# Performance work log

Hardware: AMD Instinct MI355X
Metric: run time of the kernel (lower is better)

Reference implementation:

```python
import jax, jax.numpy as jnp
import numpy as np

EPS = 1e-12  # torch F.normalize eps

def _l2norm(t, axis):
    n = jnp.linalg.norm(t, axis=axis, keepdims=True)
    return t / jnp.maximum(n, EPS)

def setup_inputs() -> dict:
    key = jax.random.key(0)
    ks = jax.random.split(key, 7)
    B, L, D, F, K = 16, 128, 512, 1024, 16
    return {
        "x": jax.random.normal(ks[0], (B, L, D), jnp.float32),
        "W_gate_basis": jax.random.normal(ks[1], (K, D, F), jnp.float32) * (1.0 / np.sqrt(D)),
        "W_up_basis": jax.random.normal(ks[2], (K, D, F), jnp.float32) * (1.0 / np.sqrt(D)),
        "W_down_basis": jax.random.normal(ks[3], (K, F, D), jnp.float32) * (1.0 / np.sqrt(F)),
        "token_coef1": jax.random.normal(ks[4], (L, K), jnp.float32),
        "token_coef2": jax.random.normal(ks[5], (L, K), jnp.float32),
        "token_coef3": jax.random.normal(ks[6], (L, K), jnp.float32),
        "u_scale_param": jnp.ones((1, F), jnp.float32),
        "v_scale_param": jnp.ones((1, F), jnp.float32),
    }

def reference(x, W_gate_basis, W_up_basis, W_down_basis,
              token_coef1, token_coef2, token_coef3,
              u_scale_param, v_scale_param):
    D = x.shape[-1]
    c1 = jax.nn.softmax(token_coef1, axis=-1)
    c2 = jax.nn.softmax(token_coef2, axis=-1)
    c3 = jax.nn.softmax(token_coef3, axis=-1)
    # per-token weights [L, D, F] / [L, F, D]
    W_gate = jnp.einsum('lk,kio->lio', c1, W_gate_basis)
    W_up = jnp.einsum('lk,kio->lio', c2, W_up_basis)
    W_down = jnp.einsum('lk,koj->loj', c3, W_down_basis)
    W_gate = _l2norm(W_gate, axis=1)   # normalize over input dim D
    W_up = _l2norm(W_up, axis=1)
    W_down = _l2norm(W_down, axis=1)   # normalize over hidden dim F
    u = jnp.einsum('bld,ldf->blf', x, W_gate)
    v = jnp.einsum('bld,ldf->blf', x, W_up)
    u_scale = jnp.abs(u_scale_param) * 1.0
    v_scale = jnp.abs(v_scale_param) * jnp.sqrt(jnp.float32(D))
    h = jax.nn.silu(v_scale * v) * (u_scale * u)
    out = jnp.einsum('blf,lfd->bld', h, W_down)
    return _l2norm(out, axis=-1)
```

## Files before the change

kernel.cpp:

```cpp
#include <hip/hip_runtime.h>
#include <hip/hip_bf16.h>
#include <cmath>


typedef _Float16 half8 __attribute__((ext_vector_type(8)));
typedef _Float16 half4 __attribute__((ext_vector_type(4)));
typedef float    f32x4 __attribute__((ext_vector_type(4)));

#define MFMA_F16 __builtin_amdgcn_mfma_f32_16x16x32_f16

static constexpr size_t OFF_P1 = 0;
static constexpr size_t OFF_P2 = 16777216;
static constexpr size_t OFF_P3 = 33554432;
static constexpr size_t OFF_HP = 50331648;
static constexpr size_t WS_FAST = OFF_HP + 4194304;

__global__ __launch_bounds__(256) void prep_basis_all(
    const float* __restrict__ wg, const float* __restrict__ wu,
    const float* __restrict__ wd,
    _Float16* __restrict__ P1, _Float16* __restrict__ P2,
    _Float16* __restrict__ P3)
{
    int z = blockIdx.y;
    const float* src = (z == 0) ? wg : (z == 1) ? wu : wd;
    _Float16*    dst = (z == 0) ? P1 : (z == 1) ? P2 : P3;
    int A  = (z == 2) ? 1024 : 512;
    int Bd = (z == 2) ? 512 : 1024;
    int nb = Bd >> 6;
    int a0 = (blockIdx.x / nb) * 4;
    int b0 = (blockIdx.x % nb) * 64;

    __shared__ __align__(16) float S[16 * 257];
    int tid = threadIdx.x;
#pragma unroll
    for (int k = 0; k < 16; ++k)
        S[k * 257 + tid] =
            src[(size_t)k * A * Bd + (size_t)(a0 + (tid >> 6)) * Bd + b0 + (tid & 63)];
    __syncthreads();

    int a = tid >> 6, b = tid & 63;
    const float* col = &S[tid];
    half8 v0, v1;
#pragma unroll
    for (int k = 0; k < 8; ++k) v0[k] = (_Float16)col[k * 257];
#pragma unroll
    for (int k = 0; k < 8; ++k) v1[k] = (_Float16)col[(k + 8) * 257];
    _Float16* out = dst + ((size_t)(a0 + a) * Bd + (b0 + b)) * 16;
    *(half8*)out       = v0;
    *(half8*)(out + 8) = v1;
}

__global__ __launch_bounds__(256) void up_fast(
    const _Float16* __restrict__ P1, const _Float16* __restrict__ P2,
    const float* __restrict__ x,
    const float* __restrict__ tc1, const float* __restrict__ tc2,
    const float* __restrict__ usp, const float* __restrict__ vsp,
    _Float16* __restrict__ Hp)
{
    int lg = blockIdx.x >> 6;
    int f0 = (blockIdx.x & 63) * 16;
    int tid = threadIdx.x;
    int w = tid >> 6, lane = tid & 63;
    int n = lane & 15, kc = lane >> 4;

    __shared__ __align__(16) _Float16 Bh[2][32 * 264];
    __shared__ __align__(16) _Float16 Wt[2][16 * 648];
    __shared__ float CN[2 * 256];

    if (tid < 32) {
        int s = tid >> 4, ll = tid & 15;
        const float* row = (s ? tc2 : tc1) + (size_t)(lg * 16 + ll) * 16;
        float e[16], m = -1e30f, sum = 0.f;
#pragma unroll
        for (int k = 0; k < 16; ++k) m = fmaxf(m, row[k]);
#pragma unroll
        for (int k = 0; k < 16; ++k) { e[k] = __expf(row[k] - m); sum += e[k]; }
        float r = 1.f / sum;
#pragma unroll
        for (int k = 0; k < 16; ++k) CN[s * 256 + ll * 16 + k] = e[k] * r;
    }
    __syncthreads();

    half8 cf1 = { 0, 0, 0, 0, 0, 0, 0, 0 };
    half8 cf2 = { 0, 0, 0, 0, 0, 0, 0, 0 };
    if (kc < 2) {
#pragma unroll
        for (int j = 0; j < 8; ++j) {
            cf1[j] = (_Float16)CN[0 * 256 + n * 16 + kc * 8 + j];
            cf2[j] = (_Float16)CN[1 * 256 + n * 16 + kc * 8 + j];
        }
    }

    f32x4 zf = { 0.f, 0.f, 0.f, 0.f };
    f32x4 aU[4], aV[4];
#pragma unroll
    for (int i = 0; i < 4; ++i) { aU[i] = zf; aV[i] = zf; }
    float nsqU[4] = { 0.f, 0.f, 0.f, 0.f };
    float nsqV[4] = { 0.f, 0.f, 0.f, 0.f };
    half8 xf[4];

    for (int it = 0; it < 16; ++it) {
        int d0 = it * 32;
        if (it > 0) {
#pragma unroll
            for (int li = 0; li < 4; ++li) {
                int l = w * 4 + li;
                half8 wU = *(const half8*)(&Wt[0][l * 648 + n * 40 + kc * 8]);
                half8 wV = *(const half8*)(&Wt[1][l * 648 + n * 40 + kc * 8]);
                aU[li] = MFMA_F16(xf[li], wU, aU[li], 0, 0, 0);
                aV[li] = MFMA_F16(xf[li], wV, aV[li], 0, 0, 0);
            }
        }
#pragma unroll
        for (int m = 0; m < 2; ++m) {
            const _Float16* P = m ? P2 : P1;
#pragma unroll
            for (int i2 = 0; i2 < 4; ++i2) {
                int u = i2 * 256 + tid;
                int dd = u >> 5, seg = u & 31;
                *(half8*)(&Bh[m][dd * 264 + seg * 8]) = *(const half8*)(
                    P + ((size_t)(d0 + dd) * 1024 + f0) * 16 + seg * 8);
            }
        }
        __syncthreads();
#pragma unroll
        for (int fl = 0; fl < 4; ++fl) {
            int f_l = w * 4 + fl;
#pragma unroll
            for (int dg = 0; dg < 2; ++dg) {
                half8 a1 = { 0, 0, 0, 0, 0, 0, 0, 0 };
                half8 a2 = { 0, 0, 0, 0, 0, 0, 0, 0 };
                if (kc < 2) {
                    a1 = *(const half8*)(&Bh[0][(dg * 16 + n) * 264 + f_l * 16 + kc * 8]);
                    a2 = *(const half8*)(&Bh[1][(dg * 16 + n) * 264 + f_l * 16 + kc * 8]);
                }
                f32x4 c1 = MFMA_F16(a1, cf1, zf, 0, 0, 0);
                nsqU[fl] += c1[0] * c1[0] + c1[1] * c1[1]
                          + c1[2] * c1[2] + c1[3] * c1[3];
                half4 h1 = { (_Float16)c1[0], (_Float16)c1[1],
                             (_Float16)c1[2], (_Float16)c1[3] };
                *(half4*)(&Wt[0][n * 648 + f_l * 40 + dg * 16 + kc * 4]) = h1;
                f32x4 c2 = MFMA_F16(a2, cf2, zf, 0, 0, 0);
                nsqV[fl] += c2[0] * c2[0] + c2[1] * c2[1]
                          + c2[2] * c2[2] + c2[3] * c2[3];
                half4 h2 = { (_Float16)c2[0], (_Float16)c2[1],
                             (_Float16)c2[2], (_Float16)c2[3] };
                *(half4*)(&Wt[1][n * 648 + f_l * 40 + dg * 16 + kc * 4]) = h2;
            }
        }
#pragma unroll
        for (int li = 0; li < 4; ++li) {
            int l = lg * 16 + w * 4 + li;
            const float* xp = x + ((size_t)n * 128 + l) * 512 + d0 + kc * 8;
            f32x4 v0 = *(const f32x4*)xp;
            f32x4 v1 = *(const f32x4*)(xp + 4);
            half8 h = { (_Float16)v0[0], (_Float16)v0[1], (_Float16)v0[2],
                        (_Float16)v0[3], (_Float16)v1[0], (_Float16)v1[1],
                        (_Float16)v1[2], (_Float16)v1[3] };
            xf[li] = h;
        }
        __syncthreads();
    }
#pragma unroll
    for (int li = 0; li < 4; ++li) {
        int l = w * 4 + li;
        half8 wU = *(const half8*)(&Wt[0][l * 648 + n * 40 + kc * 8]);
        half8 wV = *(const half8*)(&Wt[1][l * 648 + n * 40 + kc * 8]);
        aU[li] = MFMA_F16(xf[li], wU, aU[li], 0, 0, 0);
        aV[li] = MFMA_F16(xf[li], wV, aV[li], 0, 0, 0);
    }

#pragma unroll
    for (int fl = 0; fl < 4; ++fl) {
        float vU = nsqU[fl], vV = nsqV[fl];
        vU += __shfl_xor(vU, 16); vU += __shfl_xor(vU, 32);
        vV += __shfl_xor(vV, 16); vV += __shfl_xor(vV, 32);
        if (kc == 0) {
            CN[0 * 256 + n * 16 + w * 4 + fl] = vU;
            CN[1 * 256 + n * 16 + w * 4 + fl] = vV;
        }
    }
    __syncthreads();

    int f = f0 + n;
    float usv = fabsf(usp[f]);
    float vsv = fabsf(vsp[f]) * 22.627416997969522f;
#pragma unroll
    for (int li = 0; li < 4; ++li) {
        int lgl = lg * 16 + w * 4 + li;
        float r1 = 1.f / fmaxf(sqrtf(CN[0 * 256 + (w * 4 + li) * 16 + n]), 1e-12f);
        float r2 = 1.f / fmaxf(sqrtf(CN[1 * 256 + (w * 4 + li) * 16 + n]), 1e-12f);
#pragma unroll
        for (int i = 0; i < 4; ++i) {
            float u = aU[li][i] * r1;
            float v = aV[li][i] * r2;
            float zz = vsv * v;
            float sil = zz / (1.f + __expf(-zz));
            float h = sil * (usv * u);
            Hp[((size_t)lgl * 16 + kc * 4 + i) * 1024 + f] = (_Float16)h;
        }
    }
}

__global__ __launch_bounds__(256) void down_fast(
    const _Float16* __restrict__ P3, const float* __restrict__ tc3,
    const _Float16* __restrict__ Hp,
    float* __restrict__ Rp, float* __restrict__ Np)
{
    int zh = blockIdx.x >> 8;
    int rem = blockIdx.x & 255;
    int lg = rem >> 5;
    int d0 = (rem & 31) * 16;
    int tid = threadIdx.x;
    int w = tid >> 6, lane = tid & 63;
    int n = lane & 15, kc = lane >> 4;

    __shared__ __align__(16) _Float16 Bh[32 * 264];
    __shared__ __align__(16) _Float16 Wt[16 * 648];
    __shared__ float CN[256];

    if (tid < 16) {
        const float* row = tc3 + (size_t)(lg * 16 + tid) * 16;
        float e[16], m = -1e30f, sum = 0.f;
#pragma unroll
        for (int k = 0; k < 16; ++k) m = fmaxf(m, row[k]);
#pragma unroll
        for (int k = 0; k < 16; ++k) { e[k] = __expf(row[k] - m); sum += e[k]; }
        float r = 1.f / sum;
#pragma unroll
        for (int k = 0; k < 16; ++k) CN[tid * 16 + k] = e[k] * r;
    }
    __syncthreads();

    half8 cf3 = { 0, 0, 0, 0, 0, 0, 0, 0 };
    if (kc < 2) {
#pragma unroll
        for (int j = 0; j < 8; ++j)
            cf3[j] = (_Float16)CN[n * 16 + kc * 8 + j];
    }

    f32x4 zf = { 0.f, 0.f, 0.f, 0.f };
    f32x4 aO[4];
#pragma unroll
    for (int i = 0; i < 4; ++i) aO[i] = zf;
    float nsqD[4] = { 0.f, 0.f, 0.f, 0.f };
    half8 hf[4];

    for (int it = 0; it < 16; ++it) {
        int f0 = zh * 512 + it * 32;
        if (it > 0) {
#pragma unroll
            for (int li = 0; li < 4; ++li) {
                int l = w * 4 + li;
                half8 wf = *(const half8*)(&Wt[l * 648 + n * 40 + kc * 8]);
                aO[li] = MFMA_F16(hf[li], wf, aO[li], 0, 0, 0);
            }
        }
#pragma unroll
        for (int i2 = 0; i2 < 4; ++i2) {
            int u = i2 * 256 + tid;
            int ff = u >> 5, seg = u & 31;
            *(half8*)(&Bh[ff * 264 + seg * 8]) = *(const half8*)(
                P3 + ((size_t)(f0 + ff) * 512 + d0) * 16 + seg * 8);
        }
        __syncthreads();
#pragma unroll
        for (int dl = 0; dl < 4; ++dl) {
            int d_l = w * 4 + dl;
#pragma unroll
            for (int fg = 0; fg < 2; ++fg) {
                half8 a = { 0, 0, 0, 0, 0, 0, 0, 0 };
                if (kc < 2)
                    a = *(const half8*)(&Bh[(fg * 16 + n) * 264 + d_l * 16 + kc * 8]);
                f32x4 cw = MFMA_F16(a, cf3, zf, 0, 0, 0);
                nsqD[dl] += cw[0] * cw[0] + cw[1] * cw[1]
                          + cw[2] * cw[2] + cw[3] * cw[3];
                half4 h4 = { (_Float16)cw[0], (_Float16)cw[1],
                             (_Float16)cw[2], (_Float16)cw[3] };
                *(half4*)(&Wt[n * 648 + d_l * 40 + fg * 16 + kc * 4]) = h4;
            }
        }
#pragma unroll
        for (int li = 0; li < 4; ++li) {
            int l = lg * 16 + w * 4 + li;
            hf[li] = *(const half8*)(Hp + ((size_t)l * 16 + n) * 1024 + f0 + kc * 8);
        }
        __syncthreads();
    }
#pragma unroll
    for (int li = 0; li < 4; ++li) {
        int l = w * 4 + li;
        half8 wf = *(const half8*)(&Wt[l * 648 + n * 40 + kc * 8]);
        aO[li] = MFMA_F16(hf[li], wf, aO[li], 0, 0, 0);
    }

#pragma unroll
    for (int dl = 0; dl < 4; ++dl) {
        float v = nsqD[dl];
        v += __shfl_xor(v, 16); v += __shfl_xor(v, 32);
        if (kc == 0)
            Np[(size_t)zh * 65536 + (size_t)(lg * 16 + n) * 512 + d0 + w * 4 + dl] = v;
    }
#pragma unroll
    for (int li = 0; li < 4; ++li) {
        int lgl = lg * 16 + w * 4 + li;
#pragma unroll
        for (int i = 0; i < 4; ++i)
            Rp[(size_t)zh * 1048576 +
               ((size_t)(kc * 4 + i) * 128 + lgl) * 512 + d0 + n] = aO[li][i];
    }
}

__global__ __launch_bounds__(128) void final_combine(
    const float* __restrict__ Rp, const float* __restrict__ Np,
    float* __restrict__ out)
{
    int rid = blockIdx.x;
    int l = rid & 127;
    int t = threadIdx.x;
    f32x4 r0 = *(const f32x4*)(Rp + (size_t)rid * 512 + t * 4);
    f32x4 r1 = *(const f32x4*)(Rp + 1048576 + (size_t)rid * 512 + t * 4);
    f32x4 n0 = *(const f32x4*)(Np + (size_t)l * 512 + t * 4);
    f32x4 n1 = *(const f32x4*)(Np + 65536 + (size_t)l * 512 + t * 4);
    f32x4 y;
#pragma unroll
    for (int j = 0; j < 4; ++j) {
        float rr = 1.f / fmaxf(sqrtf(fmaxf(n0[j] + n1[j], 0.f)), 1e-12f);
        y[j] = (r0[j] + r1[j]) * rr;
    }
    float s = y[0] * y[0] + y[1] * y[1] + y[2] * y[2] + y[3] * y[3];
#pragma unroll
    for (int off = 32; off > 0; off >>= 1) s += __shfl_down(s, off);
    __shared__ float sred[2];
    if ((t & 63) == 0) sred[t >> 6] = s;
    __syncthreads();
    float rr = 1.f / fmaxf(sqrtf(sred[0] + sred[1]), 1e-12f);
    f32x4 o = { y[0] * rr, y[1] * rr, y[2] * rr, y[3] * rr };
    *(f32x4*)(out + (size_t)rid * 512 + t * 4) = o;
}

__global__ __launch_bounds__(256) void up_kernel(
    const float* __restrict__ x,
    const float* __restrict__ wg, const float* __restrict__ wu,
    const float* __restrict__ tc1, const float* __restrict__ tc2,
    const float* __restrict__ usp, const float* __restrict__ vsp,
    _Float16* __restrict__ Hp)
{
    int lg = blockIdx.x >> 6;
    int f0 = (blockIdx.x & 63) * 16;
    int tid = threadIdx.x;
    int w = tid >> 6, lane = tid & 63;
    int n = lane & 15, kc = lane >> 4;

    __shared__ __align__(16) _Float16 Xt[256 * 40];
    __shared__ __align__(16) _Float16 Bh[32 * 16 * 24];
    __shared__ __align__(16) _Float16 Wt[16 * 528];
    __shared__ float CN[2 * 16 * 16];

    if (tid < 32) {
        int s = tid >> 4, ll = tid & 15;
        const float* row = (s ? tc2 : tc1) + (size_t)(lg * 16 + ll) * 16;
        float e[16], m = -1e30f, sum = 0.f;
#pragma unroll
        for (int k = 0; k < 16; ++k) m = fmaxf(m, row[k]);
#pragma unroll
        for (int k = 0; k < 16; ++k) { e[k] = __expf(row[k] - m); sum += e[k]; }
        float r = 1.f / sum;
#pragma unroll
        for (int k = 0; k < 16; ++k) CN[s * 256 + ll * 16 + k] = e[k] * r;
    }
    __syncthreads();

    half8 cf1 = { 0, 0, 0, 0, 0, 0, 0, 0 };
    half8 cf2 = { 0, 0, 0, 0, 0, 0, 0, 0 };
    if (kc < 2) {
#pragma unroll
        for (int j = 0; j < 8; ++j) {
            cf1[j] = (_Float16)CN[0 * 256 + n * 16 + kc * 8 + j];
            cf2[j] = (_Float16)CN[1 * 256 + n * 16 + kc * 8 + j];
        }
    }

    f32x4 zf = { 0.f, 0.f, 0.f, 0.f };
    f32x4 aU[4], aV[4];
#pragma unroll
    for (int i = 0; i < 4; ++i) { aU[i] = zf; aV[i] = zf; }
    float nsqU[4] = { 0.f, 0.f, 0.f, 0.f };
    float nsqV[4] = { 0.f, 0.f, 0.f, 0.f };

    for (int it = 0; it < 16; ++it) {
        int d0 = it * 32;
#pragma unroll
        for (int p = 0; p < 8; ++p) {
            int r = p * 32 + (tid >> 3);
            int fj = tid & 7;
            int ll = r >> 4, b = r & 15;
            f32x4 v = *(const f32x4*)(
                x + ((size_t)(b * 128 + lg * 16 + ll) * 512 + d0 + fj * 4));
            half4 h = { (_Float16)v[0], (_Float16)v[1],
                        (_Float16)v[2], (_Float16)v[3] };
            *(half4*)(&Xt[r * 40 + fj * 4]) = h;
        }
#pragma unroll
        for (int p = 0; p < 8; ++p) {
            int idx = p * 256 + tid;
            int q = idx & 3, dd = (idx >> 2) & 31, k = idx >> 7;
            f32x4 v = *(const f32x4*)(
                wg + ((size_t)k * 512 + d0 + dd) * 1024 + f0 + q * 4);
#pragma unroll
            for (int j = 0; j < 4; ++j)
                Bh[(dd * 16 + q * 4 + j) * 24 + k] = (_Float16)v[j];
        }
        __syncthreads();
#pragma unroll
        for (int fl = 0; fl < 4; ++fl) {
            int f_l = w * 4 + fl;
#pragma unroll
            for (int dg = 0; dg < 2; ++dg) {
                half8 a = { 0, 0, 0, 0, 0, 0, 0, 0 };
                if (kc < 2)
                    a = *(const half8*)(&Bh[((dg * 16 + n) * 16 + f_l) * 24 + kc * 8]);
                f32x4 cw = MFMA_F16(a, cf1, zf, 0, 0, 0);
                nsqU[fl] += cw[0] * cw[0] + cw[1] * cw[1]
                          + cw[2] * cw[2] + cw[3] * cw[3];
                half4 h4 = { (_Float16)cw[0], (_Float16)cw[1],
                             (_Float16)cw[2], (_Float16)cw[3] };
                *(half4*)(&Wt[n * 528 + f_l * 32 + dg * 16 + kc * 4]) = h4;
            }
        }
        __syncthreads();
#pragma unroll
        for (int li = 0; li < 4; ++li) {
            int l = w * 4 + li;
            half8 xf = *(const half8*)(&Xt[(l * 16 + n) * 40 + kc * 8]);
            half8 wf = *(const half8*)(&Wt[l * 528 + n * 32 + kc * 8]);
            aU[li] = MFMA_F16(xf, wf, aU[li], 0, 0, 0);
        }
#pragma unroll
        for (int p = 0; p < 8; ++p) {
            int idx = p * 256 + tid;
            int q = idx & 3, dd = (idx >> 2) & 31, k = idx >> 7;
            f32x4 v = *(const f32x4*)(
                wu + ((size_t)k * 512 + d0 + dd) * 1024 + f0 + q * 4);
#pragma unroll
            for (int j = 0; j < 4; ++j)
                Bh[(dd * 16 + q * 4 + j) * 24 + k] = (_Float16)v[j];
        }
        __syncthreads();
#pragma unroll
        for (int fl = 0; fl < 4; ++fl) {
            int f_l = w * 4 + fl;
#pragma unroll
            for (int dg = 0; dg < 2; ++dg) {
                half8 a = { 0, 0, 0, 0, 0, 0, 0, 0 };
                if (kc < 2)
                    a = *(const half8*)(&Bh[((dg * 16 + n) * 16 + f_l) * 24 + kc * 8]);
                f32x4 cw = MFMA_F16(a, cf2, zf, 0, 0, 0);
                nsqV[fl] += cw[0] * cw[0] + cw[1] * cw[1]
                          + cw[2] * cw[2] + cw[3] * cw[3];
                half4 h4 = { (_Float16)cw[0], (_Float16)cw[1],
                             (_Float16)cw[2], (_Float16)cw[3] };
                *(half4*)(&Wt[n * 528 + f_l * 32 + dg * 16 + kc * 4]) = h4;
            }
        }
        __syncthreads();
#pragma unroll
        for (int li = 0; li < 4; ++li) {
            int l = w * 4 + li;
            half8 xf = *(const half8*)(&Xt[(l * 16 + n) * 40 + kc * 8]);
            half8 wf = *(const half8*)(&Wt[l * 528 + n * 32 + kc * 8]);
            aV[li] = MFMA_F16(xf, wf, aV[li], 0, 0, 0);
        }
        __syncthreads();
    }

#pragma unroll
    for (int fl = 0; fl < 4; ++fl) {
        float vU = nsqU[fl], vV = nsqV[fl];
        vU += __shfl_xor(vU, 16); vU += __shfl_xor(vU, 32);
        vV += __shfl_xor(vV, 16); vV += __shfl_xor(vV, 32);
        if (kc == 0) {
            CN[0 * 256 + n * 16 + w * 4 + fl] = vU;
            CN[1 * 256 + n * 16 + w * 4 + fl] = vV;
        }
    }
    __syncthreads();

    int f = f0 + n;
    float usv = fabsf(usp[f]);
    float vsv = fabsf(vsp[f]) * 22.627416997969522f;
#pragma unroll
    for (int li = 0; li < 4; ++li) {
        int lgl = lg * 16 + w * 4 + li;
        float r1 = 1.f / fmaxf(sqrtf(CN[0 * 256 + (w * 4 + li) * 16 + n]), 1e-12f);
        float r2 = 1.f / fmaxf(sqrtf(CN[1 * 256 + (w * 4 + li) * 16 + n]), 1e-12f);
#pragma unroll
        for (int i = 0; i < 4; ++i) {
            float u = aU[li][i] * r1;
            float v = aV[li][i] * r2;
            float zz = vsv * v;
            float sil = zz / (1.f + __expf(-zz));
            float h = sil * (usv * u);
            Hp[((size_t)lgl * 16 + kc * 4 + i) * 1024 + f] = (_Float16)h;
        }
    }
}

__global__ __launch_bounds__(256) void down_kernel(
    const float* __restrict__ wd, const float* __restrict__ tc3,
    const _Float16* __restrict__ Hp, float* __restrict__ out)
{
    int lg = blockIdx.x >> 5;
    int d0 = (blockIdx.x & 31) * 16;
    int tid = threadIdx.x;
    int w = tid >> 6, lane = tid & 63;
    int n = lane & 15, kc = lane >> 4;

    __shared__ __align__(16) _Float16 Ht[256 * 40];
    __shared__ __align__(16) _Float16 Bh[32 * 16 * 24];
    __shared__ __align__(16) _Float16 Wt[16 * 528];
    __shared__ float CN[16 * 16];

    if (tid < 16) {
        const float* row = tc3 + (size_t)(lg * 16 + tid) * 16;
        float e[16], m = -1e30f, sum = 0.f;
#pragma unroll
        for (int k = 0; k < 16; ++k) m = fmaxf(m, row[k]);
#pragma unroll
        for (int k = 0; k < 16; ++k) { e[k] = __expf(row[k] - m); sum += e[k]; }
        float r = 1.f / sum;
#pragma unroll
        for (int k = 0; k < 16; ++k) CN[tid * 16 + k] = e[k] * r;
    }
    __syncthreads();

    half8 cf3 = { 0, 0, 0, 0, 0, 0, 0, 0 };
    if (kc < 2) {
#pragma unroll
        for (int j = 0; j < 8; ++j)
            cf3[j] = (_Float16)CN[n * 16 + kc * 8 + j];
    }

    f32x4 zf = { 0.f, 0.f, 0.f, 0.f };
    f32x4 aO[4];
#pragma unroll
    for (int i = 0; i < 4; ++i) aO[i] = zf;
    float nsqD[4] = { 0.f, 0.f, 0.f, 0.f };

    for (int it = 0; it < 32; ++it) {
        int f0 = it * 32;
#pragma unroll
        for (int p = 0; p < 8; ++p) {
            int r = p * 32 + (tid >> 3);
            int hj = tid & 7;
            int ll = r >> 4, b = r & 15;
            half4 v = *(const half4*)(
                Hp + ((size_t)(lg * 16 + ll) * 16 + b) * 1024 + f0 + hj * 4);
            *(half4*)(&Ht[r * 40 + hj * 4]) = v;
        }
#pragma unroll
        for (int p = 0; p < 8; ++p) {
            int idx = p * 256 + tid;
            int q = idx & 3, ff = (idx >> 2) & 31, k = idx >> 7;
            f32x4 v = *(const f32x4*)(
                wd + ((size_t)k * 1024 + f0 + ff) * 512 + d0 + q * 4);
#pragma unroll
            for (int j = 0; j < 4; ++j)
                Bh[(ff * 16 + q * 4 + j) * 24 + k] = (_Float16)v[j];
        }
        __syncthreads();
#pragma unroll
        for (int dl = 0; dl < 4; ++dl) {
            int d_l = w * 4 + dl;
#pragma unroll
            for (int fg = 0; fg < 2; ++fg) {
                half8 a = { 0, 0, 0, 0, 0, 0, 0, 0 };
                if (kc < 2)
                    a = *(const half8*)(&Bh[((fg * 16 + n) * 16 + d_l) * 24 + kc * 8]);
                f32x4 cw = MFMA_F16(a, cf3, zf, 0, 0, 0);
                nsqD[dl] += cw[0] * cw[0] + cw[1] * cw[1]
                          + cw[2] * cw[2] + cw[3] * cw[3];
                half4 h4 = { (_Float16)cw[0], (_Float16)cw[1],
                             (_Float16)cw[2], (_Float16)cw[3] };
                *(half4*)(&Wt[n * 528 + d_l * 32 + fg * 16 + kc * 4]) = h4;
            }
        }
        __syncthreads();
#pragma unroll
        for (int li = 0; li < 4; ++li) {
            int l = w * 4 + li;
            half8 hf = *(const half8*)(&Ht[(l * 16 + n) * 40 + kc * 8]);
            half8 wf = *(const half8*)(&Wt[l * 528 + n * 32 + kc * 8]);
            aO[li] = MFMA_F16(hf, wf, aO[li], 0, 0, 0);
        }
        __syncthreads();
    }

#pragma unroll
    for (int dl = 0; dl < 4; ++dl) {
        float v = nsqD[dl];
        v += __shfl_xor(v, 16); v += __shfl_xor(v, 32);
        if (kc == 0) CN[n * 16 + w * 4 + dl] = v;
    }
    __syncthreads();

#pragma unroll
    for (int li = 0; li < 4; ++li) {
        int lgl = lg * 16 + w * 4 + li;
        float r3 = 1.f / fmaxf(sqrtf(CN[(w * 4 + li) * 16 + n]), 1e-12f);
#pragma unroll
        for (int i = 0; i < 4; ++i)
            out[((size_t)(kc * 4 + i) * 128 + lgl) * 512 + d0 + n] = aO[li][i] * r3;
    }
}

__global__ __launch_bounds__(128) void final_kernel(float* __restrict__ out)
{
    int rid = blockIdx.x;
    int t = threadIdx.x;
    f32x4 y = *(const f32x4*)(out + (size_t)rid * 512 + t * 4);
    float s = y[0] * y[0] + y[1] * y[1] + y[2] * y[2] + y[3] * y[3];
#pragma unroll
    for (int off = 32; off > 0; off >>= 1) s += __shfl_down(s, off);
    __shared__ float sred[2];
    if ((t & 63) == 0) sred[t >> 6] = s;
    __syncthreads();
    float rr = 1.f / fmaxf(sqrtf(sred[0] + sred[1]), 1e-12f);
    f32x4 o = { y[0] * rr, y[1] * rr, y[2] * rr, y[3] * rr };
    *(f32x4*)(out + (size_t)rid * 512 + t * 4) = o;
}

extern "C" void kernel_launch(void* const* d_in, const int* in_sizes, int n_in,
                              void* d_out, int out_size, void* d_ws, size_t ws_size,
                              hipStream_t stream)
{
    (void)in_sizes; (void)n_in; (void)out_size;
    const float* x   = (const float*)d_in[0];
    const float* wg  = (const float*)d_in[1];
    const float* wu  = (const float*)d_in[2];
    const float* wd  = (const float*)d_in[3];
    const float* tc1 = (const float*)d_in[4];
    const float* tc2 = (const float*)d_in[5];
    const float* tc3 = (const float*)d_in[6];
    const float* usp = (const float*)d_in[7];
    const float* vsp = (const float*)d_in[8];
    float* outp = (float*)d_out;
    char* ws = (char*)d_ws;

    if (ws_size >= WS_FAST) {
        _Float16* P1 = (_Float16*)(ws + OFF_P1);
        _Float16* P2 = (_Float16*)(ws + OFF_P2);
        _Float16* P3 = (_Float16*)(ws + OFF_P3);
        _Float16* Hp = (_Float16*)(ws + OFF_HP);
        float* Rp = (float*)(ws + OFF_P1);
        float* Np = (float*)(ws + OFF_P2);
        prep_basis_all<<<dim3(2048, 3), dim3(256), 0, stream>>>(wg, wu, wd,
                                                                P1, P2, P3);
        up_fast<<<dim3(512), dim3(256), 0, stream>>>(P1, P2, x, tc1, tc2,
                                                     usp, vsp, Hp);
        down_fast<<<dim3(512), dim3(256), 0, stream>>>(P3, tc3, Hp, Rp, Np);
        final_combine<<<dim3(2048), dim3(128), 0, stream>>>(Rp, Np, outp);
    } else {
        _Float16* Hp = (_Float16*)ws;
        up_kernel<<<dim3(512), dim3(256), 0, stream>>>(x, wg, wu, tc1, tc2,
                                                       usp, vsp, Hp);
        down_kernel<<<dim3(256), dim3(256), 0, stream>>>(wd, tc3, Hp, outp);
        final_kernel<<<dim3(2048), dim3(128), 0, stream>>>(outp);
    }
}
```

Before: 238.7 us.

## Transpose packed basis layout, load basis fragments directly to registers, split down K into 4

The basis prep kernel now writes the packed fp16 basis with the output-feature dimension outermost. Each wave can then load its MFMA A-fragments straight from global memory into registers, and the shared-memory staging buffer and its barrier go away. The global fragment loads are issued before the previous iteration's accumulation MFMAs so their latency is hidden. The Wt padding shrinks, launch bounds request two blocks per CU, and the down kernel splits the hidden dimension four ways over twice as many blocks. final_combine now sums four partials instead of two, which adds partial-sum traffic to the workspace.

New measurement: 239.7 us. About the same (+0.4%).

```diff
diff --git a/kernel.cpp b/kernel.cpp
--- a/kernel.cpp
+++ b/kernel.cpp
@@ -45,12 +45,12 @@
     for (int k = 0; k < 8; ++k) v0[k] = (_Float16)col[k * 257];
 #pragma unroll
     for (int k = 0; k < 8; ++k) v1[k] = (_Float16)col[(k + 8) * 257];
-    _Float16* out = dst + ((size_t)(a0 + a) * Bd + (b0 + b)) * 16;
+    _Float16* out = dst + ((size_t)(b0 + b) * A + (a0 + a)) * 16;
     *(half8*)out       = v0;
     *(half8*)(out + 8) = v1;
 }
 
-__global__ __launch_bounds__(256) void up_fast(
+__global__ __launch_bounds__(256, 2) void up_fast(
     const _Float16* __restrict__ P1, const _Float16* __restrict__ P2,
     const float* __restrict__ x,
     const float* __restrict__ tc1, const float* __restrict__ tc2,
@@ -63,8 +63,7 @@
     int w = tid >> 6, lane = tid & 63;
     int n = lane & 15, kc = lane >> 4;
 
-    __shared__ __align__(16) _Float16 Bh[2][32 * 264];
-    __shared__ __align__(16) _Float16 Wt[2][16 * 648];
+    __shared__ __align__(16) _Float16 Wt[2][16 * 584];
     __shared__ float CN[2 * 256];
 
     if (tid < 32) {
@@ -98,54 +97,33 @@
     float nsqU[4] = { 0.f, 0.f, 0.f, 0.f };
     float nsqV[4] = { 0.f, 0.f, 0.f, 0.f };
     half8 xf[4];
+    half8 pa[2][4][2];
 
     for (int it = 0; it < 16; ++it) {
         int d0 = it * 32;
+#pragma unroll
+        for (int m = 0; m < 2; ++m) {
+            const _Float16* P = m ? P2 : P1;
+#pragma unroll
+            for (int fl = 0; fl < 4; ++fl) {
+#pragma unroll
+                for (int dg = 0; dg < 2; ++dg) {
+                    half8 a = { 0, 0, 0, 0, 0, 0, 0, 0 };
+                    if (kc < 2)
+                        a = *(const half8*)(P +
+                            ((size_t)(f0 + w * 4 + fl) * 512 + d0 + dg * 16 + n) * 16 + kc * 8);
+                    pa[m][fl][dg] = a;
+                }
+            }
+        }
         if (it > 0) {
 #pragma unroll
             for (int li = 0; li < 4; ++li) {
                 int l = w * 4 + li;
-                half8 wU = *(const half8*)(&Wt[0][l * 648 + n * 40 + kc * 8]);
-                half8 wV = *(const half8*)(&Wt[1][l * 648 + n * 40 + kc * 8]);
+                half8 wU = *(const half8*)(&Wt[0][l * 584 + n * 36 + kc * 8]);
+                half8 wV = *(const half8*)(&Wt[1][l * 584 + n * 36 + kc * 8]);
                 aU[li] = MFMA_F16(xf[li], wU, aU[li], 0, 0, 0);
                 aV[li] = MFMA_F16(xf[li], wV, aV[li], 0, 0, 0);
-            }
-        }
-#pragma unroll
-        for (int m = 0; m < 2; ++m) {
-            const _Float16* P = m ? P2 : P1;
-#pragma unroll
-            for (int i2 = 0; i2 < 4; ++i2) {
-                int u = i2 * 256 + tid;
-                int dd = u >> 5, seg = u & 31;
-                *(half8*)(&Bh[m][dd * 264 + seg * 8]) = *(const half8*)(
-                    P + ((size_t)(d0 + dd) * 1024 + f0) * 16 + seg * 8);
-            }
-        }
-        __syncthreads();
-#pragma unroll
-        for (int fl = 0; fl < 4; ++fl) {
-            int f_l = w * 4 + fl;
-#pragma unroll
-            for (int dg = 0; dg < 2; ++dg) {
-                half8 a1 = { 0, 0, 0, 0, 0, 0, 0, 0 };
-                half8 a2 = { 0, 0, 0, 0, 0, 0, 0, 0 };
-                if (kc < 2) {
-                    a1 = *(const half8*)(&Bh[0][(dg * 16 + n) * 264 + f_l * 16 + kc * 8]);
-                    a2 = *(const half8*)(&Bh[1][(dg * 16 + n) * 264 + f_l * 16 + kc * 8]);
-                }
-                f32x4 c1 = MFMA_F16(a1, cf1, zf, 0, 0, 0);
-                nsqU[fl] += c1[0] * c1[0] + c1[1] * c1[1]
-                          + c1[2] * c1[2] + c1[3] * c1[3];
-                half4 h1 = { (_Float16)c1[0], (_Float16)c1[1],
-                             (_Float16)c1[2], (_Float16)c1[3] };
-                *(half4*)(&Wt[0][n * 648 + f_l * 40 + dg * 16 + kc * 4]) = h1;
-                f32x4 c2 = MFMA_F16(a2, cf2, zf, 0, 0, 0);
-                nsqV[fl] += c2[0] * c2[0] + c2[1] * c2[1]
-                          + c2[2] * c2[2] + c2[3] * c2[3];
-                half4 h2 = { (_Float16)c2[0], (_Float16)c2[1],
-                             (_Float16)c2[2], (_Float16)c2[3] };
-                *(half4*)(&Wt[1][n * 648 + f_l * 40 + dg * 16 + kc * 4]) = h2;
             }
         }
 #pragma unroll
@@ -160,12 +138,32 @@
             xf[li] = h;
         }
         __syncthreads();
+#pragma unroll
+        for (int fl = 0; fl < 4; ++fl) {
+            int f_l = w * 4 + fl;
+#pragma unroll
+            for (int dg = 0; dg < 2; ++dg) {
+                f32x4 c1 = MFMA_F16(pa[0][fl][dg], cf1, zf, 0, 0, 0);
+                nsqU[fl] += c1[0] * c1[0] + c1[1] * c1[1]
+                          + c1[2] * c1[2] + c1[3] * c1[3];
+                half4 h1 = { (_Float16)c1[0], (_Float16)c1[1],
+                             (_Float16)c1[2], (_Float16)c1[3] };
+                *(half4*)(&Wt[0][n * 584 + f_l * 36 + dg * 16 + kc * 4]) = h1;
+                f32x4 c2 = MFMA_F16(pa[1][fl][dg], cf2, zf, 0, 0, 0);
+                nsqV[fl] += c2[0] * c2[0] + c2[1] * c2[1]
+                          + c2[2] * c2[2] + c2[3] * c2[3];
+                half4 h2 = { (_Float16)c2[0], (_Float16)c2[1],
+                             (_Float16)c2[2], (_Float16)c2[3] };
+                *(half4*)(&Wt[1][n * 584 + f_l * 36 + dg * 16 + kc * 4]) = h2;
+            }
+        }
+        __syncthreads();
     }
 #pragma unroll
     for (int li = 0; li < 4; ++li) {
         int l = w * 4 + li;
-        half8 wU = *(const half8*)(&Wt[0][l * 648 + n * 40 + kc * 8]);
-        half8 wV = *(const half8*)(&Wt[1][l * 648 + n * 40 + kc * 8]);
+        half8 wU = *(const half8*)(&Wt[0][l * 584 + n * 36 + kc * 8]);
+        half8 wV = *(const half8*)(&Wt[1][l * 584 + n * 36 + kc * 8]);
         aU[li] = MFMA_F16(xf[li], wU, aU[li], 0, 0, 0);
         aV[li] = MFMA_F16(xf[li], wV, aV[li], 0, 0, 0);
     }
@@ -202,7 +200,7 @@
     }
 }
 
-__global__ __launch_bounds__(256) void down_fast(
+__global__ __launch_bounds__(256, 2) void down_fast(
     const _Float16* __restrict__ P3, const float* __restrict__ tc3,
     const _Float16* __restrict__ Hp,
     float* __restrict__ Rp, float* __restrict__ Np)
@@ -215,8 +213,7 @@
     int w = tid >> 6, lane = tid & 63;
     int n = lane & 15, kc = lane >> 4;
 
-    __shared__ __align__(16) _Float16 Bh[32 * 264];
-    __shared__ __align__(16) _Float16 Wt[16 * 648];
+    __shared__ __align__(16) _Float16 Wt[16 * 584];
     __shared__ float CN[256];
 
     if (tid < 16) {
@@ -245,52 +242,54 @@
     for (int i = 0; i < 4; ++i) aO[i] = zf;
     float nsqD[4] = { 0.f, 0.f, 0.f, 0.f };
     half8 hf[4];
-
-    for (int it = 0; it < 16; ++it) {
-        int f0 = zh * 512 + it * 32;
-        if (it > 0) {
-#pragma unroll
-            for (int li = 0; li < 4; ++li) {
-                int l = w * 4 + li;
-                half8 wf = *(const half8*)(&Wt[l * 648 + n * 40 + kc * 8]);
-                aO[li] = MFMA_F16(hf[li], wf, aO[li], 0, 0, 0);
-            }
-        }
-#pragma unroll
-        for (int i2 = 0; i2 < 4; ++i2) {
-            int u = i2 * 256 + tid;
-            int ff = u >> 5, seg = u & 31;
-            *(half8*)(&Bh[ff * 264 + seg * 8]) = *(const half8*)(
-                P3 + ((size_t)(f0 + ff) * 512 + d0) * 16 + seg * 8);
-        }
-        __syncthreads();
+    half8 pa[4][2];
+
+    for (int it = 0; it < 8; ++it) {
+        int f0 = zh * 256 + it * 32;
 #pragma unroll
         for (int dl = 0; dl < 4; ++dl) {
-            int d_l = w * 4 + dl;
 #pragma unroll
             for (int fg = 0; fg < 2; ++fg) {
                 half8 a = { 0, 0, 0, 0, 0, 0, 0, 0 };
                 if (kc < 2)
-                    a = *(const half8*)(&Bh[(fg * 16 + n) * 264 + d_l * 16 + kc * 8]);
-                f32x4 cw = MFMA_F16(a, cf3, zf, 0, 0, 0);
+                    a = *(const half8*)(P3 +
+                        ((size_t)(d0 + w * 4 + dl) * 1024 + f0 + fg * 16 + n) * 16 + kc * 8);
+                pa[dl][fg] = a;
+            }
+        }
+        if (it > 0) {
+#pragma unroll
+            for (int li = 0; li < 4; ++li) {
+                int l = w * 4 + li;
+                half8 wf = *(const half8*)(&Wt[l * 584 + n * 36 + kc * 8]);
+                aO[li] = MFMA_F16(hf[li], wf, aO[li], 0, 0, 0);
+            }
+        }
+#pragma unroll
+        for (int li = 0; li < 4; ++li) {
+            int l = lg * 16 + w * 4 + li;
+            hf[li] = *(const half8*)(Hp + ((size_t)l * 16 + n) * 1024 + f0 + kc * 8);
+        }
+        __syncthreads();
+#pragma unroll
+        for (int dl = 0; dl < 4; ++dl) {
+            int d_l = w * 4 + dl;
+#pragma unroll
+            for (int fg = 0; fg < 2; ++fg) {
+                f32x4 cw = MFMA_F16(pa[dl][fg], cf3, zf, 0, 0, 0);
                 nsqD[dl] += cw[0] * cw[0] + cw[1] * cw[1]
                           + cw[2] * cw[2] + cw[3] * cw[3];
                 half4 h4 = { (_Float16)cw[0], (_Float16)cw[1],
                              (_Float16)cw[2], (_Float16)cw[3] };
-                *(half4*)(&Wt[n * 648 + d_l * 40 + fg * 16 + kc * 4]) = h4;
-            }
-        }
-#pragma unroll
-        for (int li = 0; li < 4; ++li) {
-            int l = lg * 16 + w * 4 + li;
-            hf[li] = *(const half8*)(Hp + ((size_t)l * 16 + n) * 1024 + f0 + kc * 8);
+                *(half4*)(&Wt[n * 584 + d_l * 36 + fg * 16 + kc * 4]) = h4;
+            }
         }
         __syncthreads();
     }
 #pragma unroll
     for (int li = 0; li < 4; ++li) {
         int l = w * 4 + li;
-        half8 wf = *(const half8*)(&Wt[l * 648 + n * 40 + kc * 8]);
+        half8 wf = *(const half8*)(&Wt[l * 584 + n * 36 + kc * 8]);
         aO[li] = MFMA_F16(hf[li], wf, aO[li], 0, 0, 0);
     }
 
@@ -318,15 +317,20 @@
     int rid = blockIdx.x;
     int l = rid & 127;
     int t = threadIdx.x;
-    f32x4 r0 = *(const f32x4*)(Rp + (size_t)rid * 512 + t * 4);
-    f32x4 r1 = *(const f32x4*)(Rp + 1048576 + (size_t)rid * 512 + t * 4);
-    f32x4 n0 = *(const f32x4*)(Np + (size_t)l * 512 + t * 4);
-    f32x4 n1 = *(const f32x4*)(Np + 65536 + (size_t)l * 512 + t * 4);
+    f32x4 r = { 0.f, 0.f, 0.f, 0.f };
+    f32x4 nn = { 0.f, 0.f, 0.f, 0.f };
+#pragma unroll
+    for (int zh = 0; zh < 4; ++zh) {
+        f32x4 rz = *(const f32x4*)(Rp + (size_t)zh * 1048576 + (size_t)rid * 512 + t * 4);
+        f32x4 nz = *(const f32x4*)(Np + (size_t)zh * 65536 + (size_t)l * 512 + t * 4);
+#pragma unroll
+        for (int j = 0; j < 4; ++j) { r[j] += rz[j]; nn[j] += nz[j]; }
+    }
     f32x4 y;
 #pragma unroll
     for (int j = 0; j < 4; ++j) {
-        float rr = 1.f / fmaxf(sqrtf(fmaxf(n0[j] + n1[j], 0.f)), 1e-12f);
-        y[j] = (r0[j] + r1[j]) * rr;
+        float rr = 1.f / fmaxf(sqrtf(fmaxf(nn[j], 0.f)), 1e-12f);
+        y[j] = r[j] * rr;
     }
     float s = y[0] * y[0] + y[1] * y[1] + y[2] * y[2] + y[3] * y[3];
 #pragma unroll
@@ -658,7 +662,7 @@
                                                                 P1, P2, P3);
         up_fast<<<dim3(512), dim3(256), 0, stream>>>(P1, P2, x, tc1, tc2,
                                                      usp, vsp, Hp);
-        down_fast<<<dim3(512), dim3(256), 0, stream>>>(P3, tc3, Hp, Rp, Np);
+        down_fast<<<dim3(1024), dim3(256), 0, stream>>>(P3, tc3, Hp, Rp, Np);
         final_combine<<<dim3(2048), dim3(128), 0, stream>>>(Rp, Np, outp);
     } else {
         _Float16* Hp = (_Float16*)ws;
```
